# Kernel optimization log

Measured on AMD Instinct MI355X. Metric: run time of the kernel, lower is better.

The kernel has to match this reference:

```python
import jax, jax.numpy as jnp
import numpy as np

# MPO config: input_size = output_size = 4096 = 16**3, num_cores = 3, rank = 16
D_IN = 16    # in_leg_dim
D_OUT = 16   # out_leg_dim
RANK = 16
IN_SIZE = D_IN ** 3
OUT_SIZE = D_OUT ** 3
B = 2048     # flattened batch*seq tokens


def setup_inputs() -> dict:
    key = jax.random.key(0)
    ks = jax.random.split(key, 5)
    bound = 1.0 / np.sqrt(IN_SIZE)
    u = lambda k, shp: jax.random.uniform(k, shp, jnp.float32, -bound, bound)
    return {
        "x": jax.random.normal(ks[0], (B, IN_SIZE), dtype=jnp.float32),
        "first_core": u(ks[1], (D_IN, RANK, D_OUT)),        # (in, rank_right, out)
        "middle_core": u(ks[2], (D_IN, RANK, RANK, D_OUT)),  # (in, rank_left, rank_right, out)
        "last_core": u(ks[3], (D_IN, RANK, D_OUT)),          # (in, rank_left, out)
        "bias": u(ks[4], (OUT_SIZE,)),
    }


def reference(x, first_core, middle_core, last_core, bias):
    # Faithful MPO chain contraction, same edge wiring and order as the
    # tensornetwork-based original (contract input legs left-to-right,
    # threading the bond/rank index through the cores).
    xr = x.reshape(-1, D_IN, D_IN, D_IN)                       # (b, i, j, k)
    # contract input leg i with first core -> legs (b, j, k, r, m)
    t = jnp.einsum('bijk,irm->bjkrm', xr, first_core)
    # contract input leg j and bond r with middle core -> (b, k, m, s, n)
    t = jnp.einsum('bjkrm,jrsn->bkmsn', t, middle_core)
    # contract input leg k and bond s with last core -> (b, m, n, o)
    t = jnp.einsum('bkmsn,kso->bmno', t, last_core)
    return t.reshape(-1, OUT_SIZE) + bias
```

## Files before the change

kernel.cpp:

```cpp
#include <hip/hip_runtime.h>

#define DLEG 16
#define IN_SIZE 4096
#define OUT_SIZE 4096
#define BATCH 2048

#define SX 25.4f
#define SW 1.1545455e6f

typedef __attribute__((ext_vector_type(4))) int i32x4;

__device__ __forceinline__ signed char f2i8(float f, float s) {
  int q = __float2int_rn(f * s);
  q = q > 127 ? 127 : (q < -127 ? -127 : q);
  return (signed char)q;
}

__device__ __forceinline__ void async_copy16(const void* g, void* l) {
  __builtin_amdgcn_global_load_lds(
      (const __attribute__((address_space(1))) void*)g,
      (__attribute__((address_space(3))) void*)l, 16, 0, 0);
}

__global__ __launch_bounds__(256) void k_prep(
    const float* __restrict__ x, const float* __restrict__ fc,
    const float* __restrict__ mc, const float* __restrict__ lc,
    signed char* __restrict__ xi, signed char* __restrict__ wt) {
  __shared__ float fc_s[256];
  __shared__ float mc_s[4096];
  __shared__ float a_s[1024];
  const int t = threadIdx.x;

  if (blockIdx.x < 2048) {
    const int idx = blockIdx.x * 256 + t;
    const float4* xp = (const float4*)x + (size_t)idx * 4;
    union { int4 v; signed char c[16]; } u;
#pragma unroll
    for (int q = 0; q < 4; ++q) {
      const float4 f = xp[q];
      u.c[q * 4 + 0] = f2i8(f.x, SX);
      u.c[q * 4 + 1] = f2i8(f.y, SX);
      u.c[q * 4 + 2] = f2i8(f.z, SX);
      u.c[q * 4 + 3] = f2i8(f.w, SX);
    }
    ((int4*)xi)[idx] = u.v;
    return;
  }

  const int idx = blockIdx.x - 2048;
  const int b = idx & 255;
  const int mg = idx >> 8;
  const int i = b >> 4, j = b & 15;

  fc_s[t] = fc[i * 256 + t];
#pragma unroll
  for (int q = 0; q < 16; ++q) mc_s[q * 256 + t] = mc[j * 4096 + q * 256 + t];
  __syncthreads();

  {
    const int n = t >> 4, s = t & 15;
    float accm[4] = {0.f, 0.f, 0.f, 0.f};
#pragma unroll
    for (int r = 0; r < 16; ++r) {
      const float mcv = mc_s[r * 256 + s * 16 + n];
#pragma unroll
      for (int ml = 0; ml < 4; ++ml)
        accm[ml] = fmaf(fc_s[r * 16 + mg * 4 + ml], mcv, accm[ml]);
    }
#pragma unroll
    for (int ml = 0; ml < 4; ++ml) a_s[ml * 256 + n * 16 + s] = accm[ml];
  }
  __syncthreads();

  const int k = t & 15, op = (t >> 4) & 3, sel = t >> 6;
  float lcr[4][16];
#pragma unroll
  for (int oo = 0; oo < 4; ++oo)
#pragma unroll
    for (int s = 0; s < 16; ++s)
      lcr[oo][s] = lc[k * 256 + s * 16 + op * 4 + oo];

#pragma unroll
  for (int ml = 0; ml < 4; ++ml) {
#pragma unroll
    for (int nn = 0; nn < 4; ++nn) {
      const int n = sel * 4 + nn;
      const float4* ap = (const float4*)&a_s[ml * 256 + n * 16];
      float av[16];
      ((float4*)av)[0] = ap[0];
      ((float4*)av)[1] = ap[1];
      ((float4*)av)[2] = ap[2];
      ((float4*)av)[3] = ap[3];
      float accv[4] = {0.f, 0.f, 0.f, 0.f};
#pragma unroll
      for (int s = 0; s < 16; ++s) {
#pragma unroll
        for (int oo = 0; oo < 4; ++oo)
          accv[oo] = fmaf(av[s], lcr[oo][s], accv[oo]);
      }
      const size_t colbase =
          (size_t)((mg * 4 + ml) * 256 + n * 16 + op * 4);
#pragma unroll
      for (int oo = 0; oo < 4; ++oo)
        wt[(colbase + oo) * 4096 + b * 16 + k] = f2i8(accv[oo], SW);
    }
  }
}

__global__ __launch_bounds__(256, 2) void k_gemm(
    const signed char* __restrict__ X,
    const signed char* __restrict__ Wt,
    const float* __restrict__ bias,
    float* __restrict__ out) {
  __shared__ signed char As[2][128 * 128];
  __shared__ signed char Bs[2][128 * 128];

  const int t = threadIdx.x;
  const int l = t & 63, w = t >> 6;
  const int wm = w >> 1, wn = w & 1;
  const int m0 = blockIdx.y * 128, n0 = blockIdx.x * 128;

  const signed char* xg[4];
  const signed char* wg[4];
  int ldsoff[4];
#pragma unroll
  for (int u = 0; u < 4; ++u) {
    const int c = u * 256 + t;
    const int row = c >> 3;
    const int slot = (c & 7) ^ (row & 7);
    xg[u] = X + (size_t)(m0 + row) * 4096 + slot * 16;
    wg[u] = Wt + (size_t)(n0 + row) * 4096 + slot * 16;
    ldsoff[u] = c * 16;
  }

  const int arow = wm * 64 + (l & 15);
  const int brow = wn * 64 + (l & 15);
  const int lk = l >> 4;
  const int lx = l & 7;

  i32x4 acc[4][4];
#pragma unroll
  for (int a = 0; a < 4; ++a)
#pragma unroll
    for (int c = 0; c < 4; ++c) acc[a][c] = (i32x4){0, 0, 0, 0};

#pragma unroll
  for (int u = 0; u < 4; ++u) async_copy16(xg[u], As[0] + ldsoff[u]);
#pragma unroll
  for (int u = 0; u < 4; ++u) async_copy16(wg[u], Bs[0] + ldsoff[u]);

  for (int kt = 0; kt < 4096; kt += 128) {
    const int cur = (kt >> 7) & 1;
    __syncthreads();
    if (kt + 128 < 4096) {
#pragma unroll
      for (int u = 0; u < 4; ++u)
        async_copy16(xg[u] + kt + 128, As[cur ^ 1] + ldsoff[u]);
#pragma unroll
      for (int u = 0; u < 4; ++u)
        async_copy16(wg[u] + kt + 128, Bs[cur ^ 1] + ldsoff[u]);
    }

#pragma unroll
    for (int ks = 0; ks < 2; ++ks) {
      const int slot = ((ks * 4 + lk) ^ lx) * 16;
      i32x4 af[4], bf[4];
#pragma unroll
      for (int mi = 0; mi < 4; ++mi)
        af[mi] = *(const i32x4*)&As[cur][(arow + mi * 16) * 128 + slot];
#pragma unroll
      for (int ni = 0; ni < 4; ++ni)
        bf[ni] = *(const i32x4*)&Bs[cur][(brow + ni * 16) * 128 + slot];
#pragma unroll
      for (int mi = 0; mi < 4; ++mi)
#pragma unroll
        for (int ni = 0; ni < 4; ++ni)
          acc[mi][ni] = __builtin_amdgcn_mfma_i32_16x16x64_i8(
              af[mi], bf[ni], acc[mi][ni], 0, 0, 0);
    }
  }

  const float inv = 1.0f / (SX * SW);
#pragma unroll
  for (int ni = 0; ni < 4; ++ni) {
    const int col = n0 + wn * 64 + ni * 16 + (l & 15);
    const float bv = bias[col];
#pragma unroll
    for (int mi = 0; mi < 4; ++mi) {
      const int row = m0 + wm * 64 + mi * 16 + (l >> 4) * 4;
#pragma unroll
      for (int r = 0; r < 4; ++r)
        out[(size_t)(row + r) * 4096 + col] =
            (float)acc[mi][ni][r] * inv + bv;
    }
  }
}

extern "C" void kernel_launch(void* const* d_in, const int* in_sizes, int n_in,
                              void* d_out, int out_size, void* d_ws,
                              size_t ws_size, hipStream_t stream) {
  const float* x    = (const float*)d_in[0];
  const float* fc   = (const float*)d_in[1];
  const float* mc   = (const float*)d_in[2];
  const float* lc   = (const float*)d_in[3];
  const float* bias = (const float*)d_in[4];
  float* out = (float*)d_out;

  signed char* xi = (signed char*)d_ws;
  signed char* wt = xi + (size_t)BATCH * IN_SIZE;

  k_prep<<<2048 + 1024, 256, 0, stream>>>(x, fc, mc, lc, xi, wt);
  k_gemm<<<dim3(OUT_SIZE / 128, BATCH / 128), 256, 0, stream>>>(xi, wt, bias, out);
}
```

Before: 142.9 us.

## Restructure int8 GEMM into a 128x256 tile with triple-buffered interleaved loads

The int8 MFMA GEMM now uses a 128x256 output tile with 512 threads (8 waves) and a three-stage LDS ring instead of two stages. Async global-to-LDS copies for the next-but-one K tile are split into small pieces and placed between MFMA groups. Explicit waitcnt, s_barrier, sched_barrier and setprio calls pin the schedule so loads overlap compute and waves favour MFMA issue. The cost is about 144KB of LDS per block, which allows only one block per CU, half as many blocks in the grid, and more barriers per K tile.

```diff
diff --git a/kernel.cpp b/kernel.cpp
--- a/kernel.cpp
+++ b/kernel.cpp
@@ -107,30 +107,115 @@
   }
 }
 
-__global__ __launch_bounds__(256, 2) void k_gemm(
+
+#define LG0                                              \
+  asm volatile("s_waitcnt lgkmcnt(0)" ::: "memory");     \
+  __builtin_amdgcn_sched_barrier(0)
+
+#define DS_A(KS)                                                    \
+  {                                                                 \
+    const int slot_ = (((KS) * 4 + lk) ^ lx) * 16;                  \
+    af[0] = *(const i32x4*)&Ar[(arow + 0) * 128 + slot_];           \
+    af[1] = *(const i32x4*)&Ar[(arow + 16) * 128 + slot_];          \
+    af[2] = *(const i32x4*)&Ar[(arow + 32) * 128 + slot_];          \
+    af[3] = *(const i32x4*)&Ar[(arow + 48) * 128 + slot_];          \
+  }
+
+#define DS_B2(KS, N0, N1)                                           \
+  {                                                                 \
+    const int slot_ = (((KS) * 4 + lk) ^ lx) * 16;                  \
+    bf[N0] = *(const i32x4*)&Br[(brow + (N0) * 16) * 128 + slot_];  \
+    bf[N1] = *(const i32x4*)&Br[(brow + (N1) * 16) * 128 + slot_];  \
+  }
+
+#define MFMA8(N0, N1)                                                           \
+  __builtin_amdgcn_s_setprio(1);                                                \
+  acc[0][N0] = __builtin_amdgcn_mfma_i32_16x16x64_i8(af[0], bf[N0], acc[0][N0], 0, 0, 0); \
+  acc[0][N1] = __builtin_amdgcn_mfma_i32_16x16x64_i8(af[0], bf[N1], acc[0][N1], 0, 0, 0); \
+  acc[1][N0] = __builtin_amdgcn_mfma_i32_16x16x64_i8(af[1], bf[N0], acc[1][N0], 0, 0, 0); \
+  acc[1][N1] = __builtin_amdgcn_mfma_i32_16x16x64_i8(af[1], bf[N1], acc[1][N1], 0, 0, 0); \
+  acc[2][N0] = __builtin_amdgcn_mfma_i32_16x16x64_i8(af[2], bf[N0], acc[2][N0], 0, 0, 0); \
+  acc[2][N1] = __builtin_amdgcn_mfma_i32_16x16x64_i8(af[2], bf[N1], acc[2][N1], 0, 0, 0); \
+  acc[3][N0] = __builtin_amdgcn_mfma_i32_16x16x64_i8(af[3], bf[N0], acc[3][N0], 0, 0, 0); \
+  acc[3][N1] = __builtin_amdgcn_mfma_i32_16x16x64_i8(af[3], bf[N1], acc[3][N1], 0, 0, 0); \
+  __builtin_amdgcn_s_setprio(0);                                                \
+  __builtin_amdgcn_sched_barrier(0)
+
+#define TILE(VN, DOSTAGE)                                           \
+  {                                                                 \
+    \
+    if (DOSTAGE) {                                                  \
+      async_copy16(xg[0] + ktS, Aw + xoff[0]);                      \
+      async_copy16(xg[1] + ktS, Aw + xoff[1]);                      \
+    }                                                               \
+    asm volatile("s_waitcnt vmcnt(" #VN ")" ::: "memory");          \
+    __builtin_amdgcn_s_barrier();                                   \
+    DS_A(0);                                                        \
+    DS_B2(0, 0, 1);                                                 \
+    LG0;                                                            \
+    MFMA8(0, 1);                                                    \
+    __builtin_amdgcn_s_barrier();                                   \
+                     \
+    DS_B2(0, 2, 3);                                                 \
+    if (DOSTAGE) {                                                  \
+      async_copy16(wg[0] + ktS, Bw + woff[0]);                      \
+      async_copy16(wg[1] + ktS, Bw + woff[1]);                      \
+    }                                                               \
+    __builtin_amdgcn_s_barrier();                                   \
+    LG0;                                                            \
+    MFMA8(2, 3);                                                    \
+    __builtin_amdgcn_s_barrier();                                   \
+                     \
+    DS_A(1);                                                        \
+    DS_B2(1, 0, 1);                                                 \
+    if (DOSTAGE) {                                                  \
+      async_copy16(wg[2] + ktS, Bw + woff[2]);                      \
+      async_copy16(wg[3] + ktS, Bw + woff[3]);                      \
+    }                                                               \
+    __builtin_amdgcn_s_barrier();                                   \
+    LG0;                                                            \
+    MFMA8(0, 1);                                                    \
+    __builtin_amdgcn_s_barrier();                                   \
+                                       \
+    DS_B2(1, 2, 3);                                                 \
+    __builtin_amdgcn_s_barrier();                                   \
+    LG0;                                                            \
+    MFMA8(2, 3);                                                    \
+    __builtin_amdgcn_s_barrier();                                   \
+  }
+
+__global__ __launch_bounds__(512, 2) void k_gemm(
     const signed char* __restrict__ X,
     const signed char* __restrict__ Wt,
     const float* __restrict__ bias,
     float* __restrict__ out) {
-  __shared__ signed char As[2][128 * 128];
-  __shared__ signed char Bs[2][128 * 128];
+  __shared__ __align__(16) signed char As[3][128 * 128];
+  __shared__ __align__(16) signed char Bs[3][256 * 128];
 
   const int t = threadIdx.x;
   const int l = t & 63, w = t >> 6;
-  const int wm = w >> 1, wn = w & 1;
-  const int m0 = blockIdx.y * 128, n0 = blockIdx.x * 128;
-
-  const signed char* xg[4];
-  const signed char* wg[4];
-  int ldsoff[4];
-#pragma unroll
-  for (int u = 0; u < 4; ++u) {
-    const int c = u * 256 + t;
+  const int wm = w >> 2, wn = w & 3;
+  const int m0 = blockIdx.y * 128, n0 = blockIdx.x * 256;
+
+  const signed char* xg[2];
+  int xoff[2];
+#pragma unroll
+  for (int u = 0; u < 2; ++u) {
+    const int c = u * 512 + t;
     const int row = c >> 3;
     const int slot = (c & 7) ^ (row & 7);
     xg[u] = X + (size_t)(m0 + row) * 4096 + slot * 16;
+    xoff[u] = c * 16;
+  }
+  const signed char* wg[4];
+  int woff[4];
+#pragma unroll
+  for (int u = 0; u < 4; ++u) {
+    const int c = u * 512 + t;
+    const int row = c >> 3;
+    const int slot = (c & 7) ^ (row & 7);
     wg[u] = Wt + (size_t)(n0 + row) * 4096 + slot * 16;
-    ldsoff[u] = c * 16;
+    woff[u] = c * 16;
   }
 
   const int arow = wm * 64 + (l & 15);
@@ -145,40 +230,36 @@
     for (int c = 0; c < 4; ++c) acc[a][c] = (i32x4){0, 0, 0, 0};
 
 #pragma unroll
-  for (int u = 0; u < 4; ++u) async_copy16(xg[u], As[0] + ldsoff[u]);
-#pragma unroll
-  for (int u = 0; u < 4; ++u) async_copy16(wg[u], Bs[0] + ldsoff[u]);
-
-  for (int kt = 0; kt < 4096; kt += 128) {
-    const int cur = (kt >> 7) & 1;
-    __syncthreads();
-    if (kt + 128 < 4096) {
-#pragma unroll
-      for (int u = 0; u < 4; ++u)
-        async_copy16(xg[u] + kt + 128, As[cur ^ 1] + ldsoff[u]);
-#pragma unroll
-      for (int u = 0; u < 4; ++u)
-        async_copy16(wg[u] + kt + 128, Bs[cur ^ 1] + ldsoff[u]);
-    }
-
-#pragma unroll
-    for (int ks = 0; ks < 2; ++ks) {
-      const int slot = ((ks * 4 + lk) ^ lx) * 16;
-      i32x4 af[4], bf[4];
-#pragma unroll
-      for (int mi = 0; mi < 4; ++mi)
-        af[mi] = *(const i32x4*)&As[cur][(arow + mi * 16) * 128 + slot];
-#pragma unroll
-      for (int ni = 0; ni < 4; ++ni)
-        bf[ni] = *(const i32x4*)&Bs[cur][(brow + ni * 16) * 128 + slot];
-#pragma unroll
-      for (int mi = 0; mi < 4; ++mi)
-#pragma unroll
-        for (int ni = 0; ni < 4; ++ni)
-          acc[mi][ni] = __builtin_amdgcn_mfma_i32_16x16x64_i8(
-              af[mi], bf[ni], acc[mi][ni], 0, 0, 0);
-    }
-  }
+  for (int u = 0; u < 2; ++u) async_copy16(xg[u], As[0] + xoff[u]);
+#pragma unroll
+  for (int u = 0; u < 4; ++u) async_copy16(wg[u], Bs[0] + woff[u]);
+#pragma unroll
+  for (int u = 0; u < 2; ++u) async_copy16(xg[u] + 128, As[1] + xoff[u]);
+#pragma unroll
+  for (int u = 0; u < 4; ++u) async_copy16(wg[u] + 128, Bs[1] + woff[u]);
+
+  i32x4 af[4], bf[4];
+  signed char *Ar, *Br, *Aw = As[2], *Bw = Bs[2];
+
+  int rb = 0;
+  int ktS = 256;
+#pragma unroll 1
+  for (int tt = 0; tt < 30; ++tt) {
+    const int sb = rb >= 1 ? rb - 1 : 2;
+    Ar = As[rb];
+    Br = Bs[rb];
+    Aw = As[sb];
+    Bw = Bs[sb];
+    TILE(8, 1);
+    rb = rb == 2 ? 0 : rb + 1;
+    ktS += 128;
+  }
+  Ar = As[0];
+  Br = Bs[0];
+  TILE(6, 0);
+  Ar = As[1];
+  Br = Bs[1];
+  TILE(0, 0);
 
   const float inv = 1.0f / (SX * SW);
 #pragma unroll
@@ -210,5 +291,6 @@
   signed char* wt = xi + (size_t)BATCH * IN_SIZE;
 
   k_prep<<<2048 + 1024, 256, 0, stream>>>(x, fc, mc, lc, xi, wt);
-  k_gemm<<<dim3(OUT_SIZE / 128, BATCH / 128), 256, 0, stream>>>(xi, wt, bias, out);
-}
+  k_gemm<<<dim3(OUT_SIZE / 256, BATCH / 128), 512, 0, stream>>>(xi, wt, bias,
+                                                                out);
+}
```

New measurement: 158.3 us. 10.7% more time.

## Widen int8 GEMM tile to 128x256 with 8 waves and triple-buffered LDS

Applied to the files above, without the earlier changes.

The GEMM block tile grows from 128x128 to 128x256 and the block from 4 to 8 waves. This improves operand reuse per LDS load and gives a 256-block grid. The K loop now keeps three LDS stages with explicit vmcnt waits, so two tiles are in flight. Fragments for both k-substeps are loaded before the next stage is issued, and the MFMA block runs at raised wave priority. In exchange, the kernel uses about 144KB of LDS per block, which limits occupancy to one block per CU. Register pressure also rises from holding double fragment sets.

```diff
diff --git a/kernel.cpp b/kernel.cpp
--- a/kernel.cpp
+++ b/kernel.cpp
@@ -107,30 +107,78 @@
   }
 }
 
-__global__ __launch_bounds__(256, 2) void k_gemm(
+
+#define MFMA16(AF, BF)                                                        \
+  _Pragma("unroll") for (int mi = 0; mi < 4; ++mi)                            \
+      _Pragma("unroll") for (int ni = 0; ni < 4; ++ni)                        \
+          acc[mi][ni] = __builtin_amdgcn_mfma_i32_16x16x64_i8(                \
+              AF[mi], BF[ni], acc[mi][ni], 0, 0, 0)
+
+#define LOAD_FRAGS                                                            \
+  {                                                                           \
+    const int s0 = (lk ^ lx) * 16;                                            \
+    const int s1 = ((4 + lk) ^ lx) * 16;                                      \
+    _Pragma("unroll") for (int mi = 0; mi < 4; ++mi)                          \
+        af0[mi] = *(const i32x4*)&Ar[(arow + mi * 16) * 128 + s0];            \
+    _Pragma("unroll") for (int ni = 0; ni < 4; ++ni)                          \
+        bf0[ni] = *(const i32x4*)&Br[(brow + ni * 16) * 128 + s0];            \
+    _Pragma("unroll") for (int mi = 0; mi < 4; ++mi)                          \
+        af1[mi] = *(const i32x4*)&Ar[(arow + mi * 16) * 128 + s1];            \
+    _Pragma("unroll") for (int ni = 0; ni < 4; ++ni)                          \
+        bf1[ni] = *(const i32x4*)&Br[(brow + ni * 16) * 128 + s1];            \
+  }
+
+#define STAGE6                                                                \
+  async_copy16(xg[0] + ktS, Aw + xoff[0]);                                    \
+  async_copy16(xg[1] + ktS, Aw + xoff[1]);                                    \
+  async_copy16(wg[0] + ktS, Bw + woff[0]);                                    \
+  async_copy16(wg[1] + ktS, Bw + woff[1]);                                    \
+  async_copy16(wg[2] + ktS, Bw + woff[2]);                                    \
+  async_copy16(wg[3] + ktS, Bw + woff[3])
+
+#define TILE_BODY(VN, DOSTAGE)                                                \
+  asm volatile("s_waitcnt vmcnt(" #VN ")" ::: "memory");                      \
+  __builtin_amdgcn_s_barrier();                                               \
+  __builtin_amdgcn_sched_barrier(0);                                          \
+  LOAD_FRAGS;                                                                 \
+  if (DOSTAGE) { STAGE6; }                                                    \
+  __builtin_amdgcn_s_setprio(1);                                              \
+  MFMA16(af0, bf0);                                                           \
+  MFMA16(af1, bf1);                                                           \
+  __builtin_amdgcn_s_setprio(0)
+
+__global__ __launch_bounds__(512, 2) void k_gemm(
     const signed char* __restrict__ X,
     const signed char* __restrict__ Wt,
     const float* __restrict__ bias,
     float* __restrict__ out) {
-  __shared__ signed char As[2][128 * 128];
-  __shared__ signed char Bs[2][128 * 128];
+  __shared__ __align__(16) signed char As[3][128 * 128];
+  __shared__ __align__(16) signed char Bs[3][256 * 128];
 
   const int t = threadIdx.x;
   const int l = t & 63, w = t >> 6;
-  const int wm = w >> 1, wn = w & 1;
-  const int m0 = blockIdx.y * 128, n0 = blockIdx.x * 128;
-
-  const signed char* xg[4];
-  const signed char* wg[4];
-  int ldsoff[4];
-#pragma unroll
-  for (int u = 0; u < 4; ++u) {
-    const int c = u * 256 + t;
+  const int wm = w >> 2, wn = w & 3;
+  const int m0 = blockIdx.y * 128, n0 = blockIdx.x * 256;
+
+  const signed char* xg[2];
+  int xoff[2];
+#pragma unroll
+  for (int u = 0; u < 2; ++u) {
+    const int c = u * 512 + t;
     const int row = c >> 3;
     const int slot = (c & 7) ^ (row & 7);
     xg[u] = X + (size_t)(m0 + row) * 4096 + slot * 16;
+    xoff[u] = c * 16;
+  }
+  const signed char* wg[4];
+  int woff[4];
+#pragma unroll
+  for (int u = 0; u < 4; ++u) {
+    const int c = u * 512 + t;
+    const int row = c >> 3;
+    const int slot = (c & 7) ^ (row & 7);
     wg[u] = Wt + (size_t)(n0 + row) * 4096 + slot * 16;
-    ldsoff[u] = c * 16;
+    woff[u] = c * 16;
   }
 
   const int arow = wm * 64 + (l & 15);
@@ -145,40 +193,29 @@
     for (int c = 0; c < 4; ++c) acc[a][c] = (i32x4){0, 0, 0, 0};
 
 #pragma unroll
-  for (int u = 0; u < 4; ++u) async_copy16(xg[u], As[0] + ldsoff[u]);
-#pragma unroll
-  for (int u = 0; u < 4; ++u) async_copy16(wg[u], Bs[0] + ldsoff[u]);
-
-  for (int kt = 0; kt < 4096; kt += 128) {
-    const int cur = (kt >> 7) & 1;
-    __syncthreads();
-    if (kt + 128 < 4096) {
-#pragma unroll
-      for (int u = 0; u < 4; ++u)
-        async_copy16(xg[u] + kt + 128, As[cur ^ 1] + ldsoff[u]);
-#pragma unroll
-      for (int u = 0; u < 4; ++u)
-        async_copy16(wg[u] + kt + 128, Bs[cur ^ 1] + ldsoff[u]);
-    }
-
-#pragma unroll
-    for (int ks = 0; ks < 2; ++ks) {
-      const int slot = ((ks * 4 + lk) ^ lx) * 16;
-      i32x4 af[4], bf[4];
-#pragma unroll
-      for (int mi = 0; mi < 4; ++mi)
-        af[mi] = *(const i32x4*)&As[cur][(arow + mi * 16) * 128 + slot];
-#pragma unroll
-      for (int ni = 0; ni < 4; ++ni)
-        bf[ni] = *(const i32x4*)&Bs[cur][(brow + ni * 16) * 128 + slot];
-#pragma unroll
-      for (int mi = 0; mi < 4; ++mi)
-#pragma unroll
-        for (int ni = 0; ni < 4; ++ni)
-          acc[mi][ni] = __builtin_amdgcn_mfma_i32_16x16x64_i8(
-              af[mi], bf[ni], acc[mi][ni], 0, 0, 0);
-    }
-  }
+  for (int u = 0; u < 2; ++u) async_copy16(xg[u], As[0] + xoff[u]);
+#pragma unroll
+  for (int u = 0; u < 4; ++u) async_copy16(wg[u], Bs[0] + woff[u]);
+#pragma unroll
+  for (int u = 0; u < 2; ++u) async_copy16(xg[u] + 128, As[1] + xoff[u]);
+#pragma unroll
+  for (int u = 0; u < 4; ++u) async_copy16(wg[u] + 128, Bs[1] + woff[u]);
+
+  i32x4 af0[4], bf0[4], af1[4], bf1[4];
+  signed char *Ar = As[0], *An = As[1], *Aw = As[2];
+  signed char *Br = Bs[0], *Bn = Bs[1], *Bw = Bs[2];
+
+  int ktS = 256;
+#pragma unroll 1
+  for (int tt = 0; tt < 30; ++tt) {
+    TILE_BODY(6, 1);
+    ktS += 128;
+    signed char* ta = Ar; Ar = An; An = Aw; Aw = ta;
+    signed char* tb = Br; Br = Bn; Bn = Bw; Bw = tb;
+  }
+  TILE_BODY(6, 0);
+  Ar = An; Br = Bn;
+  TILE_BODY(0, 0);
 
   const float inv = 1.0f / (SX * SW);
 #pragma unroll
@@ -210,5 +247,6 @@
   signed char* wt = xi + (size_t)BATCH * IN_SIZE;
 
   k_prep<<<2048 + 1024, 256, 0, stream>>>(x, fc, mc, lc, xi, wt);
-  k_gemm<<<dim3(OUT_SIZE / 128, BATCH / 128), 256, 0, stream>>>(xi, wt, bias, out);
-}
+  k_gemm<<<dim3(OUT_SIZE / 256, BATCH / 128), 512, 0, stream>>>(xi, wt, bias,
+                                                                out);
+}
```

New measurement: 137.4 us. -3.9%, faster.

## Restructure int8 GEMM: 128x256 tiles, 4-stage LDS pipeline for B, direct-register A loads

Applied to the files above, without the earlier changes.

Reworks the int8 MFMA GEMM to use 512-thread blocks computing 128x256 output tiles, with 8 waves arranged 2x4. Only the weight operand is staged through LDS, in a 4-deep ring of async global-to-LDS copies. Activations are loaded straight from global memory into registers, double-buffered across tiles. Explicit waitcnt/barrier scheduling and s_setprio around the MFMA bursts are meant to overlap memory latency with compute and cut LDS traffic. The cost is higher register pressure, 128KB of LDS per block (which may limit occupancy), and uncoalesced per-wave global loads for A.

```diff
diff --git a/kernel.cpp b/kernel.cpp
--- a/kernel.cpp
+++ b/kernel.cpp
@@ -107,36 +107,80 @@
   }
 }
 
-__global__ __launch_bounds__(256, 2) void k_gemm(
+
+#define ALOAD(SET, KT)                                                        \
+  { _Pragma("unroll") for (int mi = 0; mi < 4; ++mi) {                        \
+      SET[mi * 2]     = *(const i32x4*)(ag[mi] + (KT));                       \
+      SET[mi * 2 + 1] = *(const i32x4*)(ag[mi] + (KT) + 64);                  \
+  } }
+
+#define BREAD(SET, BUF)                                                       \
+  { const signed char* bp = Bs0 + (BUF) * 32768;                              \
+    _Pragma("unroll") for (int ni = 0; ni < 4; ++ni) {                        \
+      SET[ni]     = *(const i32x4*)&bp[(brow + ni * 16) * 128 + s0f];         \
+      SET[4 + ni] = *(const i32x4*)&bp[(brow + ni * 16) * 128 + s1f];         \
+  } }
+
+#define STAGE_B(BUF, KT)                                                      \
+  { signed char* dp = Bs0 + (BUF) * 32768;                                    \
+    _Pragma("unroll") for (int u = 0; u < 4; ++u)                             \
+      async_copy16(wg[u] + (KT), dp + woff[u]); }
+
+#define MFMA32(ASET, BSET)                                                    \
+  __builtin_amdgcn_s_setprio(1);                                              \
+  _Pragma("unroll") for (int ks = 0; ks < 2; ++ks)                            \
+    _Pragma("unroll") for (int mi = 0; mi < 4; ++mi)                          \
+      _Pragma("unroll") for (int ni = 0; ni < 4; ++ni)                        \
+        acc[mi][ni] = __builtin_amdgcn_mfma_i32_16x16x64_i8(                  \
+            ASET[mi * 2 + ks], BSET[ks * 4 + ni], acc[mi][ni], 0, 0, 0);      \
+  __builtin_amdgcn_s_setprio(0)
+
+#define TILE(CURA, CURB, NXTA, NXTB, VN, DOSTAGE, DOLOAD)                     \
+  if (DOSTAGE) { STAGE_B(((ktS >> 7) & 3), ktS); }                            \
+  if (DOLOAD)  { ALOAD(NXTA, ktA); }                                          \
+  asm volatile("s_waitcnt lgkmcnt(0)" ::: "memory");                          \
+  asm volatile("s_waitcnt vmcnt(" #VN ")" ::: "memory");                      \
+  __builtin_amdgcn_s_barrier();                                               \
+  __builtin_amdgcn_sched_barrier(0);                                          \
+  if (DOLOAD) { BREAD(NXTB, ((ktA >> 7) & 3)); }                              \
+  __builtin_amdgcn_sched_barrier(0);                                          \
+  MFMA32(CURA, CURB)
+
+__global__ __launch_bounds__(512, 2) void k_gemm(
     const signed char* __restrict__ X,
     const signed char* __restrict__ Wt,
     const float* __restrict__ bias,
     float* __restrict__ out) {
-  __shared__ signed char As[2][128 * 128];
-  __shared__ signed char Bs[2][128 * 128];
+  __shared__ __align__(16) signed char Bs[4][256 * 128];
+  signed char* Bs0 = &Bs[0][0];
 
   const int t = threadIdx.x;
   const int l = t & 63, w = t >> 6;
-  const int wm = w >> 1, wn = w & 1;
-  const int m0 = blockIdx.y * 128, n0 = blockIdx.x * 128;
-
-  const signed char* xg[4];
+  const int wm = w >> 2, wn = w & 3;
+  const int m0 = blockIdx.y * 128, n0 = blockIdx.x * 256;
+
   const signed char* wg[4];
-  int ldsoff[4];
+  int woff[4];
 #pragma unroll
   for (int u = 0; u < 4; ++u) {
-    const int c = u * 256 + t;
+    const int c = u * 512 + t;
     const int row = c >> 3;
     const int slot = (c & 7) ^ (row & 7);
-    xg[u] = X + (size_t)(m0 + row) * 4096 + slot * 16;
     wg[u] = Wt + (size_t)(n0 + row) * 4096 + slot * 16;
-    ldsoff[u] = c * 16;
-  }
-
-  const int arow = wm * 64 + (l & 15);
+    woff[u] = c * 16;
+  }
+
+  const signed char* ag[4];
+#pragma unroll
+  for (int mi = 0; mi < 4; ++mi)
+    ag[mi] = X + (size_t)(m0 + wm * 64 + (l & 15) + mi * 16) * 4096 +
+             (l >> 4) * 16;
+
   const int brow = wn * 64 + (l & 15);
   const int lk = l >> 4;
   const int lx = l & 7;
+  const int s0f = (lk ^ lx) * 16;
+  const int s1f = ((4 + lk) ^ lx) * 16;
 
   i32x4 acc[4][4];
 #pragma unroll
@@ -144,41 +188,33 @@
 #pragma unroll
     for (int c = 0; c < 4; ++c) acc[a][c] = (i32x4){0, 0, 0, 0};
 
-#pragma unroll
-  for (int u = 0; u < 4; ++u) async_copy16(xg[u], As[0] + ldsoff[u]);
-#pragma unroll
-  for (int u = 0; u < 4; ++u) async_copy16(wg[u], Bs[0] + ldsoff[u]);
-
-  for (int kt = 0; kt < 4096; kt += 128) {
-    const int cur = (kt >> 7) & 1;
-    __syncthreads();
-    if (kt + 128 < 4096) {
-#pragma unroll
-      for (int u = 0; u < 4; ++u)
-        async_copy16(xg[u] + kt + 128, As[cur ^ 1] + ldsoff[u]);
-#pragma unroll
-      for (int u = 0; u < 4; ++u)
-        async_copy16(wg[u] + kt + 128, Bs[cur ^ 1] + ldsoff[u]);
-    }
-
-#pragma unroll
-    for (int ks = 0; ks < 2; ++ks) {
-      const int slot = ((ks * 4 + lk) ^ lx) * 16;
-      i32x4 af[4], bf[4];
-#pragma unroll
-      for (int mi = 0; mi < 4; ++mi)
-        af[mi] = *(const i32x4*)&As[cur][(arow + mi * 16) * 128 + slot];
-#pragma unroll
-      for (int ni = 0; ni < 4; ++ni)
-        bf[ni] = *(const i32x4*)&Bs[cur][(brow + ni * 16) * 128 + slot];
-#pragma unroll
-      for (int mi = 0; mi < 4; ++mi)
-#pragma unroll
-        for (int ni = 0; ni < 4; ++ni)
-          acc[mi][ni] = __builtin_amdgcn_mfma_i32_16x16x64_i8(
-              af[mi], bf[ni], acc[mi][ni], 0, 0, 0);
-    }
-  }
+  i32x4 Pa[8], Pb[8], Qa[8], Qb[8];
+
+  STAGE_B(0, 0);
+  STAGE_B(1, 128);
+  STAGE_B(2, 256);
+  ALOAD(Pa, 0);
+  asm volatile("s_waitcnt vmcnt(16)" ::: "memory");
+  __builtin_amdgcn_s_barrier();
+  __builtin_amdgcn_sched_barrier(0);
+  BREAD(Pb, 0);
+
+  int ktS = 384, ktA = 128;
+  TILE(Pa, Pb, Qa, Qb, 12, 1, 1);
+  ktS += 128; ktA += 128;
+
+#pragma unroll 1
+  for (int tt = 0; tt < 14; ++tt) {
+    TILE(Qa, Qb, Pa, Pb, 12, 1, 1);
+    ktS += 128; ktA += 128;
+    TILE(Pa, Pb, Qa, Qb, 12, 1, 1);
+    ktS += 128; ktA += 128;
+  }
+  TILE(Qa, Qb, Pa, Pb, 8, 0, 1);
+  ktA += 128;
+  TILE(Pa, Pb, Qa, Qb, 8, 0, 1);
+  ktA += 128;
+  TILE(Qa, Qb, Pa, Pb, 0, 0, 0);
 
   const float inv = 1.0f / (SX * SW);
 #pragma unroll
@@ -210,5 +246,6 @@
   signed char* wt = xi + (size_t)BATCH * IN_SIZE;
 
   k_prep<<<2048 + 1024, 256, 0, stream>>>(x, fc, mc, lc, xi, wt);
-  k_gemm<<<dim3(OUT_SIZE / 128, BATCH / 128), 256, 0, stream>>>(xi, wt, bias, out);
-}
+  k_gemm<<<dim3(OUT_SIZE / 256, BATCH / 128), 512, 0, stream>>>(xi, wt, bias,
+                                                                out);
+}
```

Result: slower. 173.6 us (+21.5%).
